# Kernel optimization log

Hardware: AMD Instinct MI355X
Metric: run time of the kernel (lower is better)

Reference implementation:

```python
import jax, jax.numpy as jnp
import numpy as np
from jax import lax

KS = 5            # patch kernel size
STRIDE = 4        # patch stride / scale ratio
SHIFTS = (2, 2)   # roll shifts before patch extraction
SOFTMAX_SCALE = 10.0
MID_CH = 64
BAND_HS = 8


def same_pad(x, k, s):
    """TensorFlow-style SAME padding for kernel k, stride s (NCHW)."""
    H, W = x.shape[-2], x.shape[-1]
    oh, ow = -(-H // s), -(-W // s)
    ph = max(0, (oh - 1) * s + k - H)
    pw = max(0, (ow - 1) * s + k - W)
    return jnp.pad(x, ((0, 0), (0, 0), (ph // 2, ph - ph // 2), (pw // 2, pw - pw // 2)))


def extract_patches(x, k, s, shifts):
    """torch.nn.Unfold equivalent with SAME padding and roll -> [N, L, C, k, k]."""
    x = same_pad(x, k, s)
    x = jnp.roll(x, shifts[0], axis=2)
    x = jnp.roll(x, shifts[1], axis=3)
    p = lax.conv_general_dilated_patches(
        x, (k, k), (s, s), 'VALID', dimension_numbers=('NCHW', 'OIHW', 'NCHW'))
    N, _, Hn, Wn = p.shape
    C = x.shape[1]
    # channel ordering is (C, kh, kw) channel-slowest, matching torch unfold
    return p.reshape(N, C, k, k, Hn * Wn).transpose(0, 4, 1, 2, 3)


def conv3(x, w, b):
    """3x3 conv, padding=1, bias + LeakyReLU(0.01) (BasicBlock)."""
    y = lax.conv_general_dilated(x, w, (1, 1), [(1, 1), (1, 1)],
                                 dimension_numbers=('NCHW', 'OIHW', 'NCHW'))
    return jax.nn.leaky_relu(y + b[None, :, None, None], 0.01)


def setup_inputs() -> dict:
    key = jax.random.key(0)
    ks = jax.random.split(key, 11)
    f32 = jnp.float32
    return {
        'ms':   jax.random.normal(ks[0], (2, BAND_HS, 96, 96), f32),
        'pan':  jax.random.normal(ks[1], (2, 1, 384, 384), f32),
        'pan2': jax.random.normal(ks[2], (2, 1, 96, 96), f32),
        'wq': jax.random.normal(ks[3], (MID_CH, 1, 3, 3), f32) * 0.1,
        'bq': jax.random.normal(ks[4], (MID_CH,), f32) * 0.02,
        'wk': jax.random.normal(ks[5], (MID_CH, 1, 3, 3), f32) * 0.1,
        'bk': jax.random.normal(ks[6], (MID_CH,), f32) * 0.02,
        'wv': jax.random.normal(ks[7], (BAND_HS, BAND_HS, 3, 3), f32) * 0.1,
        'bv': jax.random.normal(ks[8], (BAND_HS,), f32) * 0.02,
        'wr': jax.random.normal(ks[9], (BAND_HS, BAND_HS, 3, 3), f32) * 0.1,
        'br': jax.random.normal(ks[10], (BAND_HS,), f32) * 0.02,
    }


def reference(ms, pan, pan2, wq, bq, wk, bk, wv, bv, wr, br):
    k_fea = conv3(pan2, wk, bk)                       # [N, mid, h, w]
    q_fea = conv3(pan, wq, bq)                        # [N, mid, H, W]
    v_fea = conv3(ms, wv, bv)                         # [N, band, h, w]

    k_patch = extract_patches(k_fea, KS, STRIDE, SHIFTS)  # [N, L, mid, ks, ks]
    v_patch = extract_patches(v_fea, KS, STRIDE, SHIFTS)  # [N, L, band, ks, ks]

    def attend(q, kp, vp):
        # q: [mid, H, W]; kp: [L, mid, ks, ks]; vp: [L, band, ks, ks]
        norms = jnp.sqrt(jnp.sum(kp * kp, axis=(1, 2, 3)))      # per-patch L2 norms
        k0 = kp / jnp.max(norms)                                # global-max normalization
        q0 = same_pad(q[None], KS, STRIDE)                      # [1, mid, Hp, Wp]
        scores = lax.conv_general_dilated(
            q0, k0, (STRIDE, STRIDE), 'VALID',
            dimension_numbers=('NCHW', 'OIHW', 'NCHW'))          # [1, L, H', W']
        attn = jax.nn.softmax(scores * SOFTMAX_SCALE, axis=1)
        # conv_transpose2d(attn, vp, stride) == dilated conv with flipped, transposed kernel
        wT = jnp.flip(vp, (2, 3)).transpose(1, 0, 2, 3)          # [band, L, ks, ks]
        out = lax.conv_general_dilated(
            attn, wT, (1, 1), [(KS - 1, KS - 1)] * 2,
            lhs_dilation=(STRIDE, STRIDE),
            dimension_numbers=('NCHW', 'OIHW', 'NCHW'))          # [1, band, Ho, Wo]
        return out[0] / 6.0

    res = jax.vmap(attend)(q_fea, k_patch, v_patch)   # [N, band, Ho, Wo]
    return conv3(res, wr, br)
```

## Files before the change

kernel.cpp:

```cpp
#include <hip/hip_runtime.h>
#include <math.h>


typedef _Float16 f16;
typedef _Float16 f16x8 __attribute__((ext_vector_type(8)));
typedef float f32x4 __attribute__((ext_vector_type(4)));

namespace csa {
constexpr int NB   = 2;
constexpr int MID  = 64;
constexpr int BAND = 8;
constexpr int HK   = 96;
constexpr int HQ   = 384;
constexpr int HQP  = 385;
constexpr int XI   = 97;
constexpr int LN   = 24;
constexpr int L    = 576;
constexpr int LP   = 640;
constexpr int PS   = 96 * 96;
constexpr int KDIM = MID * 25;
constexpr int VDIM = BAND * 25;
constexpr int MV   = 256;
constexpr int HO   = 385;
constexpr size_t QPSN = (size_t)4 * HQP * XI * MID;

constexpr size_t align256(size_t x) { return (x + 255) & ~(size_t)255; }
constexpr size_t OFF_QPS  = 0;
constexpr size_t OFF_KCL  = align256(OFF_QPS + (size_t)NB*QPSN*2);
constexpr size_t OFF_VFEA = align256(OFF_KCL + (size_t)NB*HK*HK*MID*2);
constexpr size_t OFF_N2   = align256(OFF_VFEA + (size_t)NB*BAND*HK*HK*4);
constexpr size_t OFF_SC   = align256(OFF_N2   + (size_t)NB*L*4);
constexpr size_t OFF_KM   = align256(OFF_SC   + 256);
constexpr size_t OFF_VT   = align256(OFF_KM   + (size_t)NB*LP*KDIM*2);
constexpr size_t OFF_ST   = align256(OFF_VT   + (size_t)NB*MV*L*2);
constexpr size_t OFF_AT   = align256(OFF_ST   + (size_t)NB*PS*LP*4);
constexpr size_t OFF_D    = align256(OFF_AT   + (size_t)NB*PS*L*2);
constexpr size_t OFF_RES  = align256(OFF_D    + (size_t)NB*MV*PS*4);
}
using namespace csa;

__global__ __launch_bounds__(256) void csa_convq_ps(
    const float* __restrict__ in, const float* __restrict__ w,
    const float* __restrict__ b, f16* __restrict__ out) {
  int id = blockIdx.x * 256 + threadIdx.x;
  int total = NB * 4 * HQP * XI;
  if (id >= total) return;
  int xi = id % XI;
  int t = id / XI;
  int yp = t % HQP;
  t /= HQP;
  int f = t % 4;
  int n = t / 4;
  int xp = 4 * xi + f;
  f16* op = out + (size_t)id * MID;
  if (yp >= HQ || xp >= HQ) {
    f16x8 z = {0, 0, 0, 0, 0, 0, 0, 0};
#pragma unroll
    for (int c8 = 0; c8 < 8; ++c8) *(f16x8*)(op + c8 * 8) = z;
    return;
  }
  const float* ip = in + (size_t)n * HQ * HQ;
  float p[9];
#pragma unroll
  for (int dy = 0; dy < 3; ++dy)
#pragma unroll
    for (int dx = 0; dx < 3; ++dx) {
      int yy = yp + dy - 1, xx = xp + dx - 1;
      p[dy * 3 + dx] = (yy >= 0 && yy < HQ && xx >= 0 && xx < HQ)
                           ? ip[(size_t)yy * HQ + xx] : 0.f;
    }
#pragma unroll
  for (int c8 = 0; c8 < 8; ++c8) {
    f16x8 o;
#pragma unroll
    for (int e = 0; e < 8; ++e) {
      int co = c8 * 8 + e;
      float acc = b[co];
#pragma unroll
      for (int k = 0; k < 9; ++k) acc = fmaf(p[k], w[co * 9 + k], acc);
      o[e] = (f16)(acc > 0.f ? acc : 0.01f * acc);
    }
    *(f16x8*)(op + c8 * 8) = o;
  }
}

__global__ __launch_bounds__(256) void csa_conv_cl(
    const float* __restrict__ in, const float* __restrict__ w,
    const float* __restrict__ b, f16* __restrict__ out, int H) {
  int id = blockIdx.x * 256 + threadIdx.x;
  int total = NB * H * H;
  if (id >= total) return;
  int x = id % H;
  int t = id / H;
  int y = t % H;
  int n = t / H;
  f16* op = out + (size_t)id * MID;
  const float* ip = in + (size_t)n * H * H;
  float p[9];
#pragma unroll
  for (int dy = 0; dy < 3; ++dy)
#pragma unroll
    for (int dx = 0; dx < 3; ++dx) {
      int yy = y + dy - 1, xx = x + dx - 1;
      p[dy * 3 + dx] = (yy >= 0 && yy < H && xx >= 0 && xx < H)
                           ? ip[(size_t)yy * H + xx] : 0.f;
    }
#pragma unroll
  for (int c8 = 0; c8 < 8; ++c8) {
    f16x8 o;
#pragma unroll
    for (int e = 0; e < 8; ++e) {
      int co = c8 * 8 + e;
      float acc = b[co];
#pragma unroll
      for (int k = 0; k < 9; ++k) acc = fmaf(p[k], w[co * 9 + k], acc);
      o[e] = (f16)(acc > 0.f ? acc : 0.01f * acc);
    }
    *(f16x8*)(op + c8 * 8) = o;
  }
}

__global__ __launch_bounds__(256) void csa_conv3_8x8(
    const float* __restrict__ in, const float* __restrict__ w,
    const float* __restrict__ b, float* __restrict__ out, int H, int W) {
  int id = blockIdx.x * 256 + threadIdx.x;
  int total = NB * H * W;
  if (id >= total) return;
  int x = id % W;
  int t = id / W;
  int y = t % H;
  int n = t / H;
  const float* ip = in + (size_t)n * BAND * H * W;
  float p[BAND][9];
#pragma unroll
  for (int ci = 0; ci < BAND; ++ci)
#pragma unroll
    for (int dy = 0; dy < 3; ++dy)
#pragma unroll
      for (int dx = 0; dx < 3; ++dx) {
        int yy = y + dy - 1, xx = x + dx - 1;
        p[ci][dy * 3 + dx] = (yy >= 0 && yy < H && xx >= 0 && xx < W)
                                 ? ip[((size_t)ci * H + yy) * W + xx] : 0.f;
      }
  float* op = out + ((size_t)n * BAND * H + y) * W + x;
  for (int co = 0; co < BAND; ++co) {
    float acc = b[co];
#pragma unroll
    for (int ci = 0; ci < BAND; ++ci)
#pragma unroll
      for (int k = 0; k < 9; ++k)
        acc = fmaf(p[ci][k], w[(co * BAND + ci) * 9 + k], acc);
    acc = acc > 0.f ? acc : 0.01f * acc;
    op[(size_t)co * H * W] = acc;
  }
}

__global__ __launch_bounds__(256) void csa_build_patches(
    const f16* __restrict__ kcl, const float* __restrict__ v_fea,
    f16* __restrict__ Kmat, f16* __restrict__ Vt, float* __restrict__ n2) {
  int blk = blockIdx.x;
  int n = blk / LP;
  int l = blk % LP;
  int tid = threadIdx.x;
  f16* krow = Kmat + ((size_t)n * LP + l) * KDIM;
  if (l >= L) {
    f16x8 z = {0, 0, 0, 0, 0, 0, 0, 0};
    for (int ch = tid; ch < 200; ch += 256) *(f16x8*)(krow + ch * 8) = z;
    return;
  }
  int i = l / LN, j = l % LN;
  const f16* kn = kcl + (size_t)n * HK * HK * MID;
  float ss = 0.f;
  for (int ch = tid; ch < 200; ch += 256) {
    int khkw = ch >> 3;
    int c0 = (ch & 7) * 8;
    int kh = khkw / 5, kw = khkw % 5;
    int r = (4 * i + kh + 95) % 97;
    int cc = (4 * j + kw + 95) % 97;
    f16x8 v = {0, 0, 0, 0, 0, 0, 0, 0};
    if (r < HK && cc < HK)
      v = *(const f16x8*)(kn + ((size_t)r * HK + cc) * MID + c0);
#pragma unroll
    for (int e = 0; e < 8; ++e) {
      float fv = (float)v[e];
      ss += fv * fv;
    }
    *(f16x8*)(krow + ch * 8) = v;
  }
  for (int m = tid; m < MV; m += 256) {
    float v = 0.f;
    if (m < VDIM) {
      int kw = m % 5;
      int t = m / 5;
      int kh = t % 5;
      int c = t / 5;
      int r = (4 * i + kh + 95) % 97;
      int cc = (4 * j + kw + 95) % 97;
      v = (r < HK && cc < HK)
              ? v_fea[(((size_t)n * BAND + c) * HK + r) * HK + cc] : 0.f;
    }
    Vt[((size_t)n * MV + m) * L + l] = (f16)v;
  }
  __shared__ float red[256];
  red[tid] = ss;
  __syncthreads();
  for (int s = 128; s > 0; s >>= 1) {
    if (tid < s) red[tid] += red[tid + s];
    __syncthreads();
  }
  if (tid == 0) n2[n * L + l] = red[0];
}

__global__ __launch_bounds__(256) void csa_max_scale(
    const float* __restrict__ n2, float* __restrict__ scale) {
  int n = blockIdx.x;
  int tid = threadIdx.x;
  float m = 0.f;
  for (int l = tid; l < L; l += 256) m = fmaxf(m, n2[n * L + l]);
  __shared__ float red[256];
  red[tid] = m;
  __syncthreads();
  for (int s = 128; s > 0; s >>= 1) {
    if (tid < s) red[tid] = fmaxf(red[tid], red[tid + s]);
    __syncthreads();
  }
  if (tid == 0) scale[n] = 10.f / sqrtf(red[0]);
}

__device__ __forceinline__ void gl_lds16(const f16* g, f16* s) {
  __builtin_amdgcn_global_load_lds(
      (const __attribute__((address_space(1))) void*)g,
      (__attribute__((address_space(3))) void*)s, 16, 0, 0);
}

__global__ __launch_bounds__(256) void csa_gemm1(
    const f16* __restrict__ qps, const f16* __restrict__ Km,
    float* __restrict__ C) {
  __shared__ __attribute__((aligned(16))) f16 As[3 * 4096];
  __shared__ __attribute__((aligned(16))) f16 Bs[3 * 4096];
  const int tid = threadIdx.x;
  const int w = tid >> 6;
  const int l = tid & 63;
  const int q = l >> 4;
  const int r = l & 15;

  const int flat = blockIdx.x + 5 * (blockIdx.y + 72 * blockIdx.z);
  const int logical = (flat & 7) * 90 + (flat >> 3);
  const int bx = logical % 5;
  const int by = (logical / 5) % 72;
  const int nb = logical / 360;

  qps += (size_t)nb * QPSN;
  Km += (size_t)nb * LP * KDIM;
  C += (size_t)nb * (size_t)PS * L;
  const int bm = by * 128;
  const int bn = bx * 128;
  const int wm = (w >> 1) * 64;
  const int wn = (w & 1) * 64;

  f32x4 acc[4][4];
#pragma unroll
  for (int i = 0; i < 4; ++i)
#pragma unroll
    for (int j = 0; j < 4; ++j) {
      f32x4 z = {0.f, 0.f, 0.f, 0.f};
      acc[i][j] = z;
    }

  const int pg0 = bm + w * 16;
  const int y0 = pg0 / 96, x0 = pg0 % 96;
  const int pg1 = pg0 + 64;
  const int y1 = pg1 / 96, x1 = pg1 % 96;
  const int la = r * MID + q * 8;

  const f16* gb0 = Km + (size_t)(bn + w * 16 + r) * KDIM + q * 8;
  const f16* gb1 = gb0 + (size_t)64 * KDIM;
  const int am = (w >> 1) * 4;
  const int bnn = (w & 1) * 4;

  auto stage = [&](int t, int bi) {
    f16* bA = As + bi * 4096;
    f16* bB = Bs + bi * 4096;
    const int kh = t / 10;
    const int rem = t - kh * 10;
    const int kw = rem >> 1;
    const int half = rem & 1;
    const size_t u0 =
        (((size_t)(kw & 3) * HQP + (4 * y0 + kh)) * XI + x0 + (kw >> 2)) * MID;
    const size_t u1 =
        (((size_t)(kw & 3) * HQP + (4 * y1 + kh)) * XI + x1 + (kw >> 2)) * MID;
    const size_t oA = (size_t)half * 32 + la;
    gl_lds16(qps + u0 + oA, bA + w * 512);
    gl_lds16(qps + u1 + oA, bA + 2048 + w * 512);
    gl_lds16(gb0 + (size_t)t * 32, bB + w * 512);
    gl_lds16(gb1 + (size_t)t * 32, bB + 2048 + w * 512);
  };
  auto compute = [&](int bi) {
    const f16* bA = As + bi * 4096;
    const f16* bB = Bs + bi * 4096;
    f16x8 af[4], bf[4];
#pragma unroll
    for (int u = 0; u < 4; ++u) {
      af[u] = *(const f16x8*)&bA[(am + u) * 512 + q * 128 + r * 8];
      bf[u] = *(const f16x8*)&bB[(bnn + u) * 512 + q * 128 + r * 8];
    }
#pragma unroll
    for (int i = 0; i < 4; ++i)
#pragma unroll
      for (int j = 0; j < 4; ++j)
        acc[i][j] = __builtin_amdgcn_mfma_f32_16x16x32_f16(af[i], bf[j],
                                                           acc[i][j], 0, 0, 0);
  };

  stage(0, 0);
  stage(1, 1);
  int bi = 0;
  for (int t = 0; t < 48; ++t) {
    asm volatile("s_waitcnt vmcnt(4)" ::: "memory");
    __builtin_amdgcn_s_barrier();
    __builtin_amdgcn_sched_barrier(0);
    stage(t + 2, bi == 0 ? 2 : bi - 1);
    compute(bi);
    bi = (bi == 2) ? 0 : bi + 1;
  }
  asm volatile("s_waitcnt vmcnt(4)" ::: "memory");
  __builtin_amdgcn_s_barrier();
  __builtin_amdgcn_sched_barrier(0);
  compute(bi);
  bi = (bi == 2) ? 0 : bi + 1;
  asm volatile("s_waitcnt vmcnt(0)" ::: "memory");
  __builtin_amdgcn_s_barrier();
  __builtin_amdgcn_sched_barrier(0);
  compute(bi);

  const int cn = bn + wn + r;
#pragma unroll
  for (int i = 0; i < 4; ++i) {
    int rm = bm + wm + i * 16 + q * 4;
#pragma unroll
    for (int j = 0; j < 4; ++j) {
      int c = cn + j * 16;
      if (c < L) {
#pragma unroll
        for (int rr = 0; rr < 4; ++rr)
          C[(size_t)(rm + rr) * L + c] = acc[i][j][rr];
      }
    }
  }
}

__global__ __launch_bounds__(256) void csa_gemm_f16(
    const f16* __restrict__ A, const f16* __restrict__ Bt,
    float* __restrict__ C, int M, int N, int K,
    size_t strideA, size_t strideB, size_t strideC) {
  __shared__ __attribute__((aligned(16))) f16 As[3 * 4096];
  __shared__ __attribute__((aligned(16))) f16 Bs[3 * 4096];
  const int tid = threadIdx.x;
  const int w = tid >> 6;
  const int l = tid & 63;
  const int q = l >> 4;
  const int r = l & 15;

  const int gx = gridDim.x, gy = gridDim.y;
  const int nwg = gx * gy * gridDim.z;
  const int chunk = nwg >> 3;
  const int flat = blockIdx.x + gx * (blockIdx.y + gy * blockIdx.z);
  const int logical = (flat & 7) * chunk + (flat >> 3);
  const int my = logical % gy;
  const int nx = (logical / gy) % gx;
  const int nb = logical / (gy * gx);

  A += (size_t)nb * strideA;
  Bt += (size_t)nb * strideB;
  C += (size_t)nb * strideC;
  const int bm = my * 128;
  const int bn = nx * 128;
  const int wm = (w >> 1) * 64;
  const int wn = (w & 1) * 64;

  f32x4 acc[4][4];
#pragma unroll
  for (int i = 0; i < 4; ++i)
#pragma unroll
    for (int j = 0; j < 4; ++j) {
      f32x4 z = {0.f, 0.f, 0.f, 0.f};
      acc[i][j] = z;
    }

  const f16* ga0 = A + (size_t)(bm + w * 16 + r) * K + q * 8;
  const f16* ga1 = ga0 + (size_t)64 * K;
  const f16* gb0 = Bt + (size_t)(bn + w * 16 + r) * K + q * 8;
  const f16* gb1 = gb0 + (size_t)64 * K;
  const int am = (w >> 1) * 4;
  const int bnn = (w & 1) * 4;

  auto stage = [&](int t, int bi) {
    f16* bA = As + bi * 4096;
    f16* bB = Bs + bi * 4096;
    const size_t k0 = (size_t)t * 32;
    gl_lds16(ga0 + k0, bA + w * 512);
    gl_lds16(ga1 + k0, bA + 2048 + w * 512);
    gl_lds16(gb0 + k0, bB + w * 512);
    gl_lds16(gb1 + k0, bB + 2048 + w * 512);
  };
  auto compute = [&](int bi) {
    const f16* bA = As + bi * 4096;
    const f16* bB = Bs + bi * 4096;
    f16x8 af[4], bf[4];
#pragma unroll
    for (int u = 0; u < 4; ++u) {
      af[u] = *(const f16x8*)&bA[(am + u) * 512 + q * 128 + r * 8];
      bf[u] = *(const f16x8*)&bB[(bnn + u) * 512 + q * 128 + r * 8];
    }
#pragma unroll
    for (int i = 0; i < 4; ++i)
#pragma unroll
      for (int j = 0; j < 4; ++j)
        acc[i][j] =
            __builtin_amdgcn_mfma_f32_16x16x32_f16(af[i], bf[j], acc[i][j], 0, 0, 0);
  };

  const int NT = K >> 5;
  stage(0, 0);
  stage(1, 1);
  int bi = 0;
  for (int t = 0; t + 2 < NT; ++t) {
    asm volatile("s_waitcnt vmcnt(4)" ::: "memory");
    __builtin_amdgcn_s_barrier();
    __builtin_amdgcn_sched_barrier(0);
    stage(t + 2, bi == 0 ? 2 : bi - 1);
    compute(bi);
    bi = (bi == 2) ? 0 : bi + 1;
  }
  asm volatile("s_waitcnt vmcnt(4)" ::: "memory");
  __builtin_amdgcn_s_barrier();
  __builtin_amdgcn_sched_barrier(0);
  compute(bi);
  bi = (bi == 2) ? 0 : bi + 1;
  asm volatile("s_waitcnt vmcnt(0)" ::: "memory");
  __builtin_amdgcn_s_barrier();
  __builtin_amdgcn_sched_barrier(0);
  compute(bi);

  const int cn = bn + wn + r;
#pragma unroll
  for (int i = 0; i < 4; ++i) {
    int rm = bm + wm + i * 16 + q * 4;
#pragma unroll
    for (int j = 0; j < 4; ++j)
#pragma unroll
      for (int rr = 0; rr < 4; ++rr)
        C[(size_t)(rm + rr) * N + cn + j * 16] = acc[i][j][rr];
  }
}

__global__ __launch_bounds__(256) void csa_softmax(
    const float* __restrict__ scoresT, const float* __restrict__ scale,
    f16* __restrict__ attnT) {
  const int wv = threadIdx.x >> 6;
  const int lane = threadIdx.x & 63;
  const int p = blockIdx.x * 4 + wv;
  const int n = blockIdx.y;
  const float sc = scale[n];
  const float* row = scoresT + ((size_t)n * PS + p) * L;
  float v[9];
  float m = -1e30f;
#pragma unroll
  for (int j = 0; j < 9; ++j) {
    v[j] = row[lane + j * 64] * sc;
    m = fmaxf(m, v[j]);
  }
#pragma unroll
  for (int off = 32; off > 0; off >>= 1) m = fmaxf(m, __shfl_xor(m, off));
  float e[9], s = 0.f;
#pragma unroll
  for (int j = 0; j < 9; ++j) {
    e[j] = __expf(v[j] - m);
    s += e[j];
  }
#pragma unroll
  for (int off = 32; off > 0; off >>= 1) s += __shfl_xor(s, off);
  const float inv = 1.f / s;
  f16* orow = attnT + ((size_t)n * PS + p) * L;
#pragma unroll
  for (int j = 0; j < 9; ++j) orow[lane + j * 64] = (f16)(e[j] * inv);
}

__global__ __launch_bounds__(256) void csa_gather(
    const float* __restrict__ D, float* __restrict__ res) {
  int id = blockIdx.x * 256 + threadIdx.x;
  if (id >= NB * BAND * HO * HO) return;
  int ox = id % HO;
  int t = id / HO;
  int oy = t % HO;
  t = t / HO;
  int co = t % BAND;
  int n = t / BAND;
  const float* Dn = D + (size_t)n * MV * PS;
  float s = 0.f;
  int kh0 = oy & 3;
  int kw0 = ox & 3;
  for (int kh = kh0; kh < 5; kh += 4) {
    int y = (oy - kh) >> 2;
    if (y < 0 || y >= 96) continue;
    for (int kw = kw0; kw < 5; kw += 4) {
      int x = (ox - kw) >> 2;
      if (x < 0 || x >= 96) continue;
      s += Dn[(size_t)(co * 25 + kh * 5 + kw) * PS + y * 96 + x];
    }
  }
  res[id] = s * (1.f / 6.f);
}

extern "C" void kernel_launch(void* const* d_in, const int* in_sizes, int n_in,
                              void* d_out, int out_size, void* d_ws,
                              size_t ws_size, hipStream_t stream) {
  const float* ms   = (const float*)d_in[0];
  const float* pan  = (const float*)d_in[1];
  const float* pan2 = (const float*)d_in[2];
  const float* wq = (const float*)d_in[3];
  const float* bq = (const float*)d_in[4];
  const float* wk = (const float*)d_in[5];
  const float* bk = (const float*)d_in[6];
  const float* wv = (const float*)d_in[7];
  const float* bv = (const float*)d_in[8];
  const float* wr = (const float*)d_in[9];
  const float* br = (const float*)d_in[10];
  float* out = (float*)d_out;

  char* ws = (char*)d_ws;
  f16*   qps   = (f16*)(ws + OFF_QPS);
  f16*   kcl   = (f16*)(ws + OFF_KCL);
  float* v_fea = (float*)(ws + OFF_VFEA);
  float* n2    = (float*)(ws + OFF_N2);
  float* scale = (float*)(ws + OFF_SC);
  f16*   Kmat  = (f16*)(ws + OFF_KM);
  f16*   Vt    = (f16*)(ws + OFF_VT);
  float* scoT  = (float*)(ws + OFF_ST);
  f16*   attnT = (f16*)(ws + OFF_AT);
  float* Dm    = (float*)(ws + OFF_D);
  float* res   = (float*)(ws + OFF_RES);

  dim3 b256(256);
  csa_convq_ps<<<dim3((NB * 4 * HQP * XI + 255) / 256), b256, 0, stream>>>(
      pan, wq, bq, qps);
  csa_conv_cl<<<dim3((NB * HK * HK + 255) / 256), b256, 0, stream>>>(
      pan2, wk, bk, kcl, HK);
  csa_conv3_8x8<<<dim3((NB * HK * HK + 255) / 256), b256, 0, stream>>>(
      ms, wv, bv, v_fea, HK, HK);
  csa_build_patches<<<dim3(NB * LP), b256, 0, stream>>>(kcl, v_fea, Kmat, Vt,
                                                        n2);
  csa_max_scale<<<dim3(NB), b256, 0, stream>>>(n2, scale);

  csa_gemm1<<<dim3(LP / 128, PS / 128, NB), b256, 0, stream>>>(qps, Kmat,
                                                               scoT);

  csa_softmax<<<dim3(PS / 4, NB), b256, 0, stream>>>(scoT, scale, attnT);

  csa_gemm_f16<<<dim3(PS / 128, MV / 128, NB), b256, 0, stream>>>(
      Vt, attnT, Dm, MV, PS, L,
      (size_t)MV * L, (size_t)PS * L, (size_t)MV * PS);

  csa_gather<<<dim3((NB * BAND * HO * HO + 255) / 256), b256, 0, stream>>>(
      Dm, res);
  csa_conv3_8x8<<<dim3((NB * HO * HO + 255) / 256), b256, 0, stream>>>(
      res, wr, br, out, HO, HO);
}
```

Measured before the change: 273.3 us.

## Fuse input convs, retile second GEMM to 64-row blocks, fuse gather with final conv

The three input convolutions now run as a single launch that dispatches by block index. The second GEMM is specialised to fixed sizes with 64x128 tiles, which doubles the number of workgroups for better occupancy. The scatter-gather of the transposed convolution is fused with the final 3x3 conv through an 18x18 shared-memory halo tile, so the intermediate res buffer is never written to or read from global memory. The trade-offs are recomputed halo gathers and smaller MFMA tiles with less data reuse per block.

```diff
diff --git a/kernel.cpp b/kernel.cpp
--- a/kernel.cpp
+++ b/kernel.cpp
@@ -24,6 +24,9 @@
 constexpr int HO   = 385;
 constexpr size_t QPSN = (size_t)4 * HQP * XI * MID;
 
+constexpr int NBQ = (NB * 4 * HQP * XI + 255) / 256;
+constexpr int NBC = NB * HK * HK / 256;
+
 constexpr size_t align256(size_t x) { return (x + 255) & ~(size_t)255; }
 constexpr size_t OFF_QPS  = 0;
 constexpr size_t OFF_KCL  = align256(OFF_QPS + (size_t)NB*QPSN*2);
@@ -35,14 +38,12 @@
 constexpr size_t OFF_ST   = align256(OFF_VT   + (size_t)NB*MV*L*2);
 constexpr size_t OFF_AT   = align256(OFF_ST   + (size_t)NB*PS*LP*4);
 constexpr size_t OFF_D    = align256(OFF_AT   + (size_t)NB*PS*L*2);
-constexpr size_t OFF_RES  = align256(OFF_D    + (size_t)NB*MV*PS*4);
 }
 using namespace csa;
 
-__global__ __launch_bounds__(256) void csa_convq_ps(
+__device__ __forceinline__ void dev_convq(
     const float* __restrict__ in, const float* __restrict__ w,
-    const float* __restrict__ b, f16* __restrict__ out) {
-  int id = blockIdx.x * 256 + threadIdx.x;
+    const float* __restrict__ b, f16* __restrict__ out, int id) {
   int total = NB * 4 * HQP * XI;
   if (id >= total) return;
   int xi = id % XI;
@@ -84,10 +85,9 @@
   }
 }
 
-__global__ __launch_bounds__(256) void csa_conv_cl(
+__device__ __forceinline__ void dev_conv_cl(
     const float* __restrict__ in, const float* __restrict__ w,
-    const float* __restrict__ b, f16* __restrict__ out, int H) {
-  int id = blockIdx.x * 256 + threadIdx.x;
+    const float* __restrict__ b, f16* __restrict__ out, int H, int id) {
   int total = NB * H * H;
   if (id >= total) return;
   int x = id % H;
@@ -120,10 +120,10 @@
   }
 }
 
-__global__ __launch_bounds__(256) void csa_conv3_8x8(
+__device__ __forceinline__ void dev_conv8x8(
     const float* __restrict__ in, const float* __restrict__ w,
-    const float* __restrict__ b, float* __restrict__ out, int H, int W) {
-  int id = blockIdx.x * 256 + threadIdx.x;
+    const float* __restrict__ b, float* __restrict__ out, int H, int W,
+    int id) {
   int total = NB * H * W;
   if (id >= total) return;
   int x = id % W;
@@ -152,6 +152,24 @@
         acc = fmaf(p[ci][k], w[(co * BAND + ci) * 9 + k], acc);
     acc = acc > 0.f ? acc : 0.01f * acc;
     op[(size_t)co * H * W] = acc;
+  }
+}
+
+__global__ __launch_bounds__(256) void csa_convs(
+    const float* __restrict__ pan, const float* __restrict__ wq,
+    const float* __restrict__ bq, f16* __restrict__ qps,
+    const float* __restrict__ pan2, const float* __restrict__ wk,
+    const float* __restrict__ bk, f16* __restrict__ kcl,
+    const float* __restrict__ ms, const float* __restrict__ wv,
+    const float* __restrict__ bv, float* __restrict__ v_fea) {
+  const int bid = blockIdx.x;
+  const int tid = threadIdx.x;
+  if (bid < NBQ) {
+    dev_convq(pan, wq, bq, qps, bid * 256 + tid);
+  } else if (bid < NBQ + NBC) {
+    dev_conv_cl(pan2, wk, bk, kcl, HK, (bid - NBQ) * 256 + tid);
+  } else {
+    dev_conv8x8(ms, wv, bv, v_fea, HK, HK, (bid - NBQ - NBC) * 256 + tid);
   }
 }
 
@@ -349,11 +367,10 @@
   }
 }
 
-__global__ __launch_bounds__(256) void csa_gemm_f16(
-    const f16* __restrict__ A, const f16* __restrict__ Bt,
-    float* __restrict__ C, int M, int N, int K,
-    size_t strideA, size_t strideB, size_t strideC) {
-  __shared__ __attribute__((aligned(16))) f16 As[3 * 4096];
+__global__ __launch_bounds__(256) void csa_gemm2(
+    const f16* __restrict__ Vt, const f16* __restrict__ At,
+    float* __restrict__ D) {
+  __shared__ __attribute__((aligned(16))) f16 As[3 * 2048];
   __shared__ __attribute__((aligned(16))) f16 Bs[3 * 4096];
   const int tid = threadIdx.x;
   const int w = tid >> 6;
@@ -361,78 +378,73 @@
   const int q = l >> 4;
   const int r = l & 15;
 
-  const int gx = gridDim.x, gy = gridDim.y;
-  const int nwg = gx * gy * gridDim.z;
-  const int chunk = nwg >> 3;
-  const int flat = blockIdx.x + gx * (blockIdx.y + gy * blockIdx.z);
-  const int logical = (flat & 7) * chunk + (flat >> 3);
-  const int my = logical % gy;
-  const int nx = (logical / gy) % gx;
-  const int nb = logical / (gy * gx);
-
-  A += (size_t)nb * strideA;
-  Bt += (size_t)nb * strideB;
-  C += (size_t)nb * strideC;
-  const int bm = my * 128;
+  const int flat = blockIdx.x + 72 * (blockIdx.y + 4 * blockIdx.z);
+  const int logical = (flat & 7) * 72 + (flat >> 3);
+  const int nx = logical % 72;
+  const int my = (logical / 72) % 4;
+  const int nb = logical / 288;
+
+  const f16* A = Vt + (size_t)nb * MV * L;
+  const f16* Bt = At + (size_t)nb * (size_t)PS * L;
+  float* C = D + (size_t)nb * (size_t)MV * PS;
+  const int bm = my * 64;
   const int bn = nx * 128;
-  const int wm = (w >> 1) * 64;
+  const int wm = (w >> 1) * 32;
   const int wn = (w & 1) * 64;
 
-  f32x4 acc[4][4];
-#pragma unroll
-  for (int i = 0; i < 4; ++i)
+  f32x4 acc[2][4];
+#pragma unroll
+  for (int i = 0; i < 2; ++i)
 #pragma unroll
     for (int j = 0; j < 4; ++j) {
       f32x4 z = {0.f, 0.f, 0.f, 0.f};
       acc[i][j] = z;
     }
 
-  const f16* ga0 = A + (size_t)(bm + w * 16 + r) * K + q * 8;
-  const f16* ga1 = ga0 + (size_t)64 * K;
-  const f16* gb0 = Bt + (size_t)(bn + w * 16 + r) * K + q * 8;
-  const f16* gb1 = gb0 + (size_t)64 * K;
-  const int am = (w >> 1) * 4;
+  const f16* ga  = A + (size_t)(bm + w * 16 + r) * L + q * 8;
+  const f16* gb0 = Bt + (size_t)(bn + w * 16 + r) * L + q * 8;
+  const f16* gb1 = gb0 + (size_t)64 * L;
+  const int am = (w >> 1) * 2;
   const int bnn = (w & 1) * 4;
 
   auto stage = [&](int t, int bi) {
-    f16* bA = As + bi * 4096;
+    f16* bA = As + bi * 2048;
     f16* bB = Bs + bi * 4096;
     const size_t k0 = (size_t)t * 32;
-    gl_lds16(ga0 + k0, bA + w * 512);
-    gl_lds16(ga1 + k0, bA + 2048 + w * 512);
+    gl_lds16(ga + k0, bA + w * 512);
     gl_lds16(gb0 + k0, bB + w * 512);
     gl_lds16(gb1 + k0, bB + 2048 + w * 512);
   };
   auto compute = [&](int bi) {
-    const f16* bA = As + bi * 4096;
+    const f16* bA = As + bi * 2048;
     const f16* bB = Bs + bi * 4096;
-    f16x8 af[4], bf[4];
-#pragma unroll
-    for (int u = 0; u < 4; ++u) {
+    f16x8 af[2], bf[4];
+#pragma unroll
+    for (int u = 0; u < 2; ++u)
       af[u] = *(const f16x8*)&bA[(am + u) * 512 + q * 128 + r * 8];
+#pragma unroll
+    for (int u = 0; u < 4; ++u)
       bf[u] = *(const f16x8*)&bB[(bnn + u) * 512 + q * 128 + r * 8];
-    }
-#pragma unroll
-    for (int i = 0; i < 4; ++i)
+#pragma unroll
+    for (int i = 0; i < 2; ++i)
 #pragma unroll
       for (int j = 0; j < 4; ++j)
-        acc[i][j] =
-            __builtin_amdgcn_mfma_f32_16x16x32_f16(af[i], bf[j], acc[i][j], 0, 0, 0);
+        acc[i][j] = __builtin_amdgcn_mfma_f32_16x16x32_f16(af[i], bf[j],
+                                                           acc[i][j], 0, 0, 0);
   };
 
-  const int NT = K >> 5;
   stage(0, 0);
   stage(1, 1);
   int bi = 0;
-  for (int t = 0; t + 2 < NT; ++t) {
-    asm volatile("s_waitcnt vmcnt(4)" ::: "memory");
+  for (int t = 0; t < 16; ++t) {
+    asm volatile("s_waitcnt vmcnt(3)" ::: "memory");
     __builtin_amdgcn_s_barrier();
     __builtin_amdgcn_sched_barrier(0);
     stage(t + 2, bi == 0 ? 2 : bi - 1);
     compute(bi);
     bi = (bi == 2) ? 0 : bi + 1;
   }
-  asm volatile("s_waitcnt vmcnt(4)" ::: "memory");
+  asm volatile("s_waitcnt vmcnt(3)" ::: "memory");
   __builtin_amdgcn_s_barrier();
   __builtin_amdgcn_sched_barrier(0);
   compute(bi);
@@ -444,13 +456,13 @@
 
   const int cn = bn + wn + r;
 #pragma unroll
-  for (int i = 0; i < 4; ++i) {
+  for (int i = 0; i < 2; ++i) {
     int rm = bm + wm + i * 16 + q * 4;
 #pragma unroll
     for (int j = 0; j < 4; ++j)
 #pragma unroll
       for (int rr = 0; rr < 4; ++rr)
-        C[(size_t)(rm + rr) * N + cn + j * 16] = acc[i][j][rr];
+        C[(size_t)(rm + rr) * PS + cn + j * 16] = acc[i][j][rr];
   }
 }
 
@@ -486,30 +498,68 @@
   for (int j = 0; j < 9; ++j) orow[lane + j * 64] = (f16)(e[j] * inv);
 }
 
-__global__ __launch_bounds__(256) void csa_gather(
-    const float* __restrict__ D, float* __restrict__ res) {
-  int id = blockIdx.x * 256 + threadIdx.x;
-  if (id >= NB * BAND * HO * HO) return;
-  int ox = id % HO;
-  int t = id / HO;
-  int oy = t % HO;
-  t = t / HO;
-  int co = t % BAND;
-  int n = t / BAND;
+__global__ __launch_bounds__(256) void csa_gather_conv(
+    const float* __restrict__ D, const float* __restrict__ wr,
+    const float* __restrict__ br, float* __restrict__ out) {
+  __shared__ float rs[BAND][18][18];
+  __shared__ float wsm[BAND * BAND * 9];
+  __shared__ float brs[BAND];
+  const int tid = threadIdx.x;
+  const int n = blockIdx.z;
+  const int ty = blockIdx.y, tx = blockIdx.x;
   const float* Dn = D + (size_t)n * MV * PS;
-  float s = 0.f;
-  int kh0 = oy & 3;
-  int kw0 = ox & 3;
-  for (int kh = kh0; kh < 5; kh += 4) {
-    int y = (oy - kh) >> 2;
-    if (y < 0 || y >= 96) continue;
-    for (int kw = kw0; kw < 5; kw += 4) {
-      int x = (ox - kw) >> 2;
-      if (x < 0 || x >= 96) continue;
-      s += Dn[(size_t)(co * 25 + kh * 5 + kw) * PS + y * 96 + x];
-    }
-  }
-  res[id] = s * (1.f / 6.f);
+
+  for (int i = tid; i < BAND * BAND * 9; i += 256) wsm[i] = wr[i];
+  if (tid < BAND) brs[tid] = br[tid];
+
+  for (int idx = tid; idx < BAND * 18 * 18; idx += 256) {
+    int ci = idx / 324;
+    int rem = idx - ci * 324;
+    int yy = rem / 18;
+    int xx = rem - yy * 18;
+    int oy = ty * 16 - 1 + yy;
+    int ox = tx * 16 - 1 + xx;
+    float s = 0.f;
+    if (oy >= 0 && oy < HO && ox >= 0 && ox < HO) {
+      int kh0 = oy & 3;
+      int kw0 = ox & 3;
+      for (int kh = kh0; kh < 5; kh += 4) {
+        int y = (oy - kh) >> 2;
+        if (y < 0 || y >= 96) continue;
+        for (int kw = kw0; kw < 5; kw += 4) {
+          int x = (ox - kw) >> 2;
+          if (x < 0 || x >= 96) continue;
+          s += Dn[(size_t)(ci * 25 + kh * 5 + kw) * PS + y * 96 + x];
+        }
+      }
+      s *= (1.f / 6.f);
+    }
+    rs[ci][yy][xx] = s;
+  }
+  __syncthreads();
+
+  const int y = tid >> 4, x = tid & 15;
+  const int oy = ty * 16 + y, ox = tx * 16 + x;
+  if (oy >= HO || ox >= HO) return;
+  float p[BAND][9];
+#pragma unroll
+  for (int ci = 0; ci < BAND; ++ci)
+#pragma unroll
+    for (int dy = 0; dy < 3; ++dy)
+#pragma unroll
+      for (int dx = 0; dx < 3; ++dx)
+        p[ci][dy * 3 + dx] = rs[ci][y + dy][x + dx];
+  float* op = out + ((size_t)n * BAND * HO + oy) * HO + ox;
+  for (int co = 0; co < BAND; ++co) {
+    float acc = brs[co];
+#pragma unroll
+    for (int ci = 0; ci < BAND; ++ci)
+#pragma unroll
+      for (int k = 0; k < 9; ++k)
+        acc = fmaf(p[ci][k], wsm[(co * BAND + ci) * 9 + k], acc);
+    acc = acc > 0.f ? acc : 0.01f * acc;
+    op[(size_t)co * HO * HO] = acc;
+  }
 }
 
 extern "C" void kernel_launch(void* const* d_in, const int* in_sizes, int n_in,
@@ -539,15 +589,10 @@
   float* scoT  = (float*)(ws + OFF_ST);
   f16*   attnT = (f16*)(ws + OFF_AT);
   float* Dm    = (float*)(ws + OFF_D);
-  float* res   = (float*)(ws + OFF_RES);
 
   dim3 b256(256);
-  csa_convq_ps<<<dim3((NB * 4 * HQP * XI + 255) / 256), b256, 0, stream>>>(
-      pan, wq, bq, qps);
-  csa_conv_cl<<<dim3((NB * HK * HK + 255) / 256), b256, 0, stream>>>(
-      pan2, wk, bk, kcl, HK);
-  csa_conv3_8x8<<<dim3((NB * HK * HK + 255) / 256), b256, 0, stream>>>(
-      ms, wv, bv, v_fea, HK, HK);
+  csa_convs<<<dim3(NBQ + 2 * NBC), b256, 0, stream>>>(
+      pan, wq, bq, qps, pan2, wk, bk, kcl, ms, wv, bv, v_fea);
   csa_build_patches<<<dim3(NB * LP), b256, 0, stream>>>(kcl, v_fea, Kmat, Vt,
                                                         n2);
   csa_max_scale<<<dim3(NB), b256, 0, stream>>>(n2, scale);
@@ -557,12 +602,8 @@
 
   csa_softmax<<<dim3(PS / 4, NB), b256, 0, stream>>>(scoT, scale, attnT);
 
-  csa_gemm_f16<<<dim3(PS / 128, MV / 128, NB), b256, 0, stream>>>(
-      Vt, attnT, Dm, MV, PS, L,
-      (size_t)MV * L, (size_t)PS * L, (size_t)MV * PS);
-
-  csa_gather<<<dim3((NB * BAND * HO * HO + 255) / 256), b256, 0, stream>>>(
-      Dm, res);
-  csa_conv3_8x8<<<dim3((NB * HO * HO + 255) / 256), b256, 0, stream>>>(
-      res, wr, br, out, HO, HO);
-}
+  csa_gemm2<<<dim3(PS / 128, MV / 64, NB), b256, 0, stream>>>(Vt, attnT, Dm);
+
+  csa_gather_conv<<<dim3((HO + 15) / 16, (HO + 15) / 16, NB), b256, 0,
+                    stream>>>(Dm, wr, br, out);
+}
```

Measured after the change: 274.3 us. No clear change (+0.4%).
